# Kernel optimization log

Hardware: AMD Instinct MI355X
Metric: run time of the kernel (lower is better)

The kernel has to match this reference:

```python
import jax, jax.numpy as jnp
import numpy as np

B, S, D, H, F = 4, 1024, 2048, 16, 8192
HD = D // H  # head dim = 128
EPS = 1e-5


def layer_norm(x, w, b):
    mu = jnp.mean(x, axis=-1, keepdims=True)
    var = jnp.mean(jnp.square(x - mu), axis=-1, keepdims=True)
    return (x - mu) * jax.lax.rsqrt(var + EPS) * w + b


def setup_inputs() -> dict:
    key = jax.random.key(0)
    ks = jax.random.split(key, 12)
    s = 0.02  # realistic init scale for weights
    return {
        "x": jax.random.normal(ks[0], (B, S, D), jnp.float32),
        "attention_mask": jnp.zeros((B, 1, 1, S), jnp.float32),
        "wq": jax.random.normal(ks[1], (D, D), jnp.float32) * s,
        "bq": jax.random.normal(ks[2], (D,), jnp.float32) * s,
        "wk": jax.random.normal(ks[3], (D, D), jnp.float32) * s,
        "bk": jax.random.normal(ks[4], (D,), jnp.float32) * s,
        "wv": jax.random.normal(ks[5], (D, D), jnp.float32) * s,
        "bv": jax.random.normal(ks[6], (D,), jnp.float32) * s,
        "wo": jax.random.normal(ks[7], (D, D), jnp.float32) * s,
        "bo": jax.random.normal(ks[8], (D,), jnp.float32) * s,
        "ln1_w": jnp.ones((D,), jnp.float32),
        "ln1_b": jnp.zeros((D,), jnp.float32),
        "wi": jax.random.normal(ks[9], (F, D), jnp.float32) * s,
        "bi": jax.random.normal(ks[10], (F,), jnp.float32) * s,
        "wo2": jax.random.normal(ks[11], (D, F), jnp.float32) * s,
        "bo2": jnp.zeros((D,), jnp.float32),
        "ln2_w": jnp.ones((D,), jnp.float32),
        "ln2_b": jnp.zeros((D,), jnp.float32),
    }


def reference(x, attention_mask, wq, bq, wk, bk, wv, bv, wo, bo,
              ln1_w, ln1_b, wi, bi, wo2, bo2, ln2_w, ln2_b):
    # --- self attention ---
    q = (jnp.einsum('bsd,ed->bse', x, wq) + bq).reshape(B, S, H, HD).transpose(0, 2, 1, 3)
    k = (jnp.einsum('bsd,ed->bse', x, wk) + bk).reshape(B, S, H, HD).transpose(0, 2, 1, 3)
    v = (jnp.einsum('bsd,ed->bse', x, wv) + bv).reshape(B, S, H, HD).transpose(0, 2, 1, 3)
    scores = jnp.einsum('bhqd,bhkd->bhqk', q, k) / jnp.sqrt(jnp.float32(HD))
    scores = scores + attention_mask  # additive mask, broadcast over heads/query
    probs = jax.nn.softmax(scores, axis=-1)
    ctx = jnp.einsum('bhqk,bhkd->bhqd', probs, v)
    ctx = ctx.transpose(0, 2, 1, 3).reshape(B, S, D)
    # --- attention output: dense + bias + residual + LayerNorm ---
    attn_out = layer_norm(jnp.einsum('bsd,ed->bse', ctx, wo) + bo + x, ln1_w, ln1_b)
    # --- FFN: intermediate dense + bias, GELU, output dense + bias + residual + LN ---
    inter = jnp.einsum('bsd,fd->bsf', attn_out, wi) + bi
    h = jax.nn.gelu(inter, approximate=False)
    out = layer_norm(jnp.einsum('bsf,df->bsd', h, wo2) + bo2 + attn_out, ln2_w, ln2_b)
    return out
```

## Files before the change

### kernel.cpp

```cpp
#include <hip/hip_runtime.h>
#include <hip/hip_bf16.h>
#include <cstdint>
#include <cstddef>

typedef __attribute__((ext_vector_type(8))) short short8;
typedef __attribute__((ext_vector_type(4))) float f32x4;

#define DEV static __device__ __forceinline__

constexpr int kS = 1024, kD = 2048, kH = 16, kHD = 128, kF = 8192;
constexpr int kM = 4096;
constexpr int kDQKV = 6144;
constexpr float kEPS = 1e-5f;

constexpr size_t SZ_DD   = (size_t)kD * kD * 2;
constexpr size_t SZ_FD   = (size_t)kF * kD * 2;
constexpr size_t SZ_MD16 = (size_t)kM * kD * 2;
constexpr size_t SZ_MD32 = (size_t)kM * kD * 4;
constexpr size_t OFF_WQ  = 0;
constexpr size_t OFF_WK  = OFF_WQ + SZ_DD;
constexpr size_t OFF_WV  = OFF_WK + SZ_DD;
constexpr size_t OFF_WO  = OFF_WV + SZ_DD;
constexpr size_t OFF_WI  = OFF_WO + SZ_DD;
constexpr size_t OFF_WO2 = OFF_WI + SZ_FD;
constexpr size_t OFF_XB  = OFF_WO2 + SZ_FD;
constexpr size_t OFF_Q   = OFF_XB + SZ_MD16;
constexpr size_t OFF_H   = OFF_XB;
constexpr size_t OFF_CTX = OFF_Q + 3 * SZ_MD16;
constexpr size_t OFF_Y1  = OFF_CTX + SZ_MD16;
constexpr size_t OFF_A1B = OFF_Y1 + SZ_MD32;
constexpr size_t OFF_Y2  = OFF_A1B + SZ_MD16;
constexpr size_t WS_NEED = OFF_Y2 + SZ_MD32;

DEV void gload16(const void* g, void* l) {
  __builtin_amdgcn_global_load_lds(
      (const __attribute__((address_space(1))) unsigned int*)g,
      (__attribute__((address_space(3))) unsigned int*)l, 16, 0, 0);
}

DEV float b2f(short s) {
  union { unsigned u; float f; } x;
  x.u = ((unsigned)(unsigned short)s) << 16;
  return x.f;
}

__global__ void cvt_all(const float* __restrict__ x,  const float* __restrict__ wq,
                        const float* __restrict__ wk, const float* __restrict__ wv,
                        const float* __restrict__ bq, const float* __restrict__ bk,
                        const float* __restrict__ bv,
                        __hip_bfloat16* __restrict__ outw, float* __restrict__ bqkv) {
  constexpr int M1 = 1 << 20;
  constexpr int NW = 5 * M1;
  int stride = gridDim.x * blockDim.x;
  for (int i = blockIdx.x * blockDim.x + threadIdx.x; i < NW + 1536; i += stride) {
    if (i < NW) {
      const float* src; int off; int dst;
      if (i < 3 * M1) { src = (i < M1) ? wq : (i < 2 * M1) ? wk : wv;
                        off = i & (M1 - 1); dst = i; }
      else            { src = x; off = i - 3 * M1; dst = i + 9 * M1; }
      float4 v = reinterpret_cast<const float4*>(src)[off];
      union { ushort4 u; __hip_bfloat16 h[4]; } o;
      o.h[0] = __float2bfloat16(v.x);
      o.h[1] = __float2bfloat16(v.y);
      o.h[2] = __float2bfloat16(v.z);
      o.h[3] = __float2bfloat16(v.w);
      reinterpret_cast<ushort4*>(outw)[dst] = o.u;
    } else {
      int j = i - NW;
      const float* src = (j < 512) ? bq : (j < 1024) ? bk : bv;
      reinterpret_cast<float4*>(bqkv)[j] =
          reinterpret_cast<const float4*>(src)[j & 511];
    }
  }
}

template <int MODE>
__global__ __launch_bounds__(512, 2)
void gemm256(const __hip_bfloat16* __restrict__ A,
             const __hip_bfloat16* __restrict__ Bt,
             const float* __restrict__ bias,
             __hip_bfloat16* __restrict__ out0, __hip_bfloat16* __restrict__ out1,
             void* __restrict__ outb,
             int M, int N, int K, int kLen) {
  __shared__ __align__(16) char lds[131072];
  const int tid = threadIdx.x;
  const int lane = tid & 63, w = tid >> 6;
  const int wm = w >> 2, wn = w & 3;
  const int hw = w >> 2;
  const int lg = lane >> 4, lr = lane & 15;
  const int gy = M >> 8, gx = N >> 8;
  const int nwg = gridDim.x, orig = blockIdx.x;
  const int l = (orig & 7) * (nwg >> 3) + (orig >> 3);
  const int tilesPer = gx * gy;
  const int spl = l / tilesPer;
  const int rem = l - spl * tilesPer;
  const int bx = rem / gy, by = rem - bx * gy;
  const int m0 = by * 256, n0 = bx * 256;
  const int k0 = spl * kLen;
  const int NT = kLen >> 6;

  const char* gs[8];
  #pragma unroll
  for (int h = 0; h < 4; ++h) {
    const __hip_bfloat16* src = (h < 2) ? A : Bt;
    const int r0 = ((h < 2) ? m0 : n0) + (h & 1) * 128;
    #pragma unroll
    for (int i = 0; i < 2; ++i) {
      int c = i * 512 + tid;
      int row = c >> 3, slot = c & 7;
      gs[h * 2 + i] =
          (const char*)(src + (size_t)(r0 + row) * K + k0 + (slot ^ (row & 7)) * 8);
    }
  }

#define STAGE(P, H, TOFF)                                                          \
  {                                                                                \
    char* dstb = lds + (((H) < 2) ? 0 : 65536) + (P) * 32768 + ((H) & 1) * 16384;  \
    gload16(gs[(H) * 2 + 0] + (TOFF) * 128, dstb + (0 * 512 + tid) * 16);          \
    gload16(gs[(H) * 2 + 1] + (TOFF) * 128, dstb + (1 * 512 + tid) * 16);          \
  }

  auto ldA = [&](int P, int qm, int mr, int kk) {
    int row = qm * 128 + wm * 64 + mr * 16 + lr;
    return *reinterpret_cast<const short8*>(
        lds + P * 32768 + row * 128 + (((kk * 4 + lg) ^ (row & 7)) * 16));
  };
  auto ldB = [&](int P, int qn, int nr, int kk) {
    int row = qn * 128 + wn * 32 + nr * 16 + lr;
    return *reinterpret_cast<const short8*>(
        lds + 65536 + P * 32768 + row * 128 + (((kk * 4 + lg) ^ (row & 7)) * 16));
  };

  f32x4 acc[4][4][2] = {};

#define MFMA_HALF(p, kk, B)                                                     \
  _Pragma("unroll")                                                             \
  for (int mi = 0; mi < 4; ++mi)                                                \
    _Pragma("unroll")                                                           \
    for (int ni = 0; ni < 2; ++ni)                                              \
      acc[p][mi][ni] = __builtin_amdgcn_mfma_f32_16x16x32_bf16(                 \
          av[kk][mi], B[kk][ni], acc[p][mi][ni], 0, 0, 0);

#define WAIT_LGKM(n)                                                            \
  asm volatile("s_waitcnt lgkmcnt(" #n ")" ::: "memory");                       \
  __builtin_amdgcn_sched_barrier(0);

#define TILE_BODY(P, PF)                                                        \
  {                                                                             \
    asm volatile("s_waitcnt vmcnt(0)" ::: "memory");                            \
    __builtin_amdgcn_s_barrier();                                               \
    _Pragma("unroll")                                                           \
    for (int i = 0; i < 4; ++i) av[0][i] = ldA(P, hw, i, 0);                    \
    _Pragma("unroll")                                                           \
    for (int i = 0; i < 2; ++i) b0[0][i] = ldB(P, hw, i, 0);                    \
    _Pragma("unroll")                                                           \
    for (int i = 0; i < 4; ++i) av[1][i] = ldA(P, hw, i, 1);                    \
    _Pragma("unroll")                                                           \
    for (int i = 0; i < 2; ++i) b0[1][i] = ldB(P, hw, i, 1);                    \
    if (PF) { STAGE((P) ^ 1, 0, 1 + (P)) STAGE((P) ^ 1, 2, 1 + (P)) }           \
    WAIT_LGKM(6)                                                                \
    __builtin_amdgcn_s_setprio(1);                                              \
    MFMA_HALF(0, 0, b0)                                                         \
    WAIT_LGKM(0)                                                                \
    MFMA_HALF(0, 1, b0)                                                         \
    __builtin_amdgcn_s_setprio(0);                                              \
    _Pragma("unroll")                                                           \
    for (int i = 0; i < 2; ++i) b1[0][i] = ldB(P, 1 - hw, i, 0);                \
    _Pragma("unroll")                                                           \
    for (int i = 0; i < 2; ++i) b1[1][i] = ldB(P, 1 - hw, i, 1);                \
    if (PF) { STAGE((P) ^ 1, 3, 1 + (P)) STAGE((P) ^ 1, 1, 1 + (P)) }           \
    WAIT_LGKM(2)                                                                \
    __builtin_amdgcn_s_setprio(1);                                              \
    MFMA_HALF(1, 0, b1)                                                         \
    WAIT_LGKM(0)                                                                \
    MFMA_HALF(1, 1, b1)                                                         \
    __builtin_amdgcn_s_setprio(0);                                              \
    _Pragma("unroll")                                                           \
    for (int i = 0; i < 4; ++i) av[0][i] = ldA(P, 1 - hw, i, 0);                \
    _Pragma("unroll")                                                           \
    for (int i = 0; i < 4; ++i) av[1][i] = ldA(P, 1 - hw, i, 1);                \
    WAIT_LGKM(4)                                                                \
    __builtin_amdgcn_s_setprio(1);                                              \
    MFMA_HALF(2, 0, b1)                                                         \
    WAIT_LGKM(0)                                                                \
    MFMA_HALF(2, 1, b1)                                                         \
    __builtin_amdgcn_s_setprio(0);                                              \
    _Pragma("unroll")                                                           \
    for (int i = 0; i < 2; ++i) b0[0][i] = ldB(P, hw, i, 0);                    \
    _Pragma("unroll")                                                           \
    for (int i = 0; i < 2; ++i) b0[1][i] = ldB(P, hw, i, 1);                    \
    WAIT_LGKM(2)                                                                \
    __builtin_amdgcn_s_setprio(1);                                              \
    MFMA_HALF(3, 0, b0)                                                         \
    WAIT_LGKM(0)                                                                \
    MFMA_HALF(3, 1, b0)                                                         \
    __builtin_amdgcn_s_setprio(0);                                              \
  }

  STAGE(0, 0, 0) STAGE(0, 2, 0) STAGE(0, 3, 0) STAGE(0, 1, 0)

  for (int t2 = 0; t2 < NT; t2 += 2) {
    short8 av[2][4], b0[2][2], b1[2][2];
    TILE_BODY(0, true)
    TILE_BODY(1, (t2 + 2 < NT))
    #pragma unroll
    for (int j = 0; j < 8; ++j) gs[j] += 256;
  }
#undef TILE_BODY
#undef MFMA_HALF
#undef WAIT_LGKM
#undef STAGE

  #pragma unroll
  for (int p = 0; p < 4; ++p) {
    const int qm = (p < 2) ? hw : 1 - hw;
    const int qn = (p == 0 || p == 3) ? hw : 1 - hw;
    #pragma unroll
    for (int ni = 0; ni < 2; ++ni) {
      int col = n0 + qn * 128 + wn * 32 + ni * 16 + lr;
      float bvv = 0.f;
      if constexpr (MODE != 3) bvv = bias[col];
      #pragma unroll
      for (int mi = 0; mi < 4; ++mi) {
        int row0 = m0 + qm * 128 + wm * 64 + mi * 16 + lg * 4;
        #pragma unroll
        for (int r = 0; r < 4; ++r) {
          int row = row0 + r;
          float val = acc[p][mi][ni][r] + bvv;
          if constexpr (MODE == 0) {
            ((__hip_bfloat16*)outb)[(size_t)row * N + col] = __float2bfloat16(val);
          } else if constexpr (MODE == 2) {
            float g = 0.5f * val * (1.0f + erff(val * 0.70710678118654752f));
            ((__hip_bfloat16*)outb)[(size_t)row * N + col] = __float2bfloat16(g);
          } else {
            __hip_bfloat16* o = spl ? out1 : out0;
            o[(size_t)row * N + col] = __float2bfloat16(val);
          }
        }
      }
    }
  }
}

__global__ __launch_bounds__(512, 2)
void attn_fwd(const __hip_bfloat16* __restrict__ qkv,
              const float* __restrict__ mask,
              __hip_bfloat16* __restrict__ ctx,
              const float* __restrict__ wo,
              const float* __restrict__ wi, const float* __restrict__ wo2,
              __hip_bfloat16* __restrict__ outw ) {
  __shared__ __align__(16) char Ks[2][64 * 256];
  __shared__ __align__(16) char Vt[2][128 * 128];
  __shared__ __align__(16) char Ps[8][2048];
  const int tid = threadIdx.x, lane = tid & 63, w = tid >> 6;
  const int lg = lane >> 4, lr = lane & 15;
  const int orig = blockIdx.x;
  const int l = (orig & 7) * 32 + (orig >> 3);
  const int qp = l & 3, bh = l >> 2;
  const int b = bh >> 4, h = bh & 15;
  const int s4 = tid >> 5, hd4 = tid & 31;
  const size_t rb = (size_t)b * kS;
  const int hc = h * kHD;

  short8 qf[2][4];
  #pragma unroll
  for (int s = 0; s < 2; ++s) {
    const __hip_bfloat16* qp_ =
        qkv + (rb + qp * 256 + s * 128 + w * 16 + lr) * kDQKV + hc + lg * 8;
    #pragma unroll
    for (int kk = 0; kk < 4; ++kk)
      qf[s][kk] = *reinterpret_cast<const short8*>(qp_ + kk * 32);
  }

  auto stageK = [&](int bufi, int t) {
    #pragma unroll
    for (int i = 0; i < 2; ++i) {
      int c = i * 512 + tid;
      int row = c >> 4, slot = c & 15;
      gload16(qkv + (rb + t * 64 + row) * kDQKV + kD + hc + (slot ^ (row & 15)) * 8,
              Ks[bufi] + c * 16);
    }
  };
  union VU { uint2 u; ushort s[4]; };
  VU vr[4];
  auto loadV = [&](int t) {
    #pragma unroll
    for (int i = 0; i < 4; ++i)
      vr[i].u = *reinterpret_cast<const uint2*>(
          qkv + (rb + t * 64 + s4 * 4 + i) * kDQKV + 2 * kD + hc + hd4 * 4);
  };
  auto writeV = [&](int bufi) {
    #pragma unroll
    for (int j = 0; j < 4; ++j) {
      int hd = hd4 * 4 + j;
      ushort4 o4;
      o4.x = vr[0].s[j]; o4.y = vr[1].s[j]; o4.z = vr[2].s[j]; o4.w = vr[3].s[j];
      *reinterpret_cast<ushort4*>(
          Vt[bufi] + hd * 128 + (((s4 >> 1) ^ (hd & 7)) << 4) + ((s4 & 1) << 3)) = o4;
    }
  };
  float4 cw[4]; float4 cwo;
  auto cvLoad = [&](int t) {
    int g0 = ((orig * 16 + t) * 512 + tid) * 4;
    #pragma unroll
    for (int j = 0; j < 4; ++j) {
      int g = g0 + j;
      const float* src = (g < (4 << 20)) ? wi : wo2;
      int off = g & ((4 << 20) - 1);
      cw[j] = reinterpret_cast<const float4*>(src)[off];
    }
    int slot = (orig * 16 + t) * 512 + tid;
    if (slot < (1 << 20)) cwo = reinterpret_cast<const float4*>(wo)[slot];
  };
  auto cvStore = [&](int t) {
    int g0 = ((orig * 16 + t) * 512 + tid) * 4;
    #pragma unroll
    for (int j = 0; j < 4; ++j) {
      union { ushort4 u; __hip_bfloat16 hh[4]; } o4;
      o4.hh[0] = __float2bfloat16(cw[j].x);
      o4.hh[1] = __float2bfloat16(cw[j].y);
      o4.hh[2] = __float2bfloat16(cw[j].z);
      o4.hh[3] = __float2bfloat16(cw[j].w);
      reinterpret_cast<ushort4*>(outw)[(4 << 20) + g0 + j] = o4.u;
    }
    int slot = (orig * 16 + t) * 512 + tid;
    if (slot < (1 << 20)) {
      union { ushort4 u; __hip_bfloat16 hh[4]; } o4;
      o4.hh[0] = __float2bfloat16(cwo.x);
      o4.hh[1] = __float2bfloat16(cwo.y);
      o4.hh[2] = __float2bfloat16(cwo.z);
      o4.hh[3] = __float2bfloat16(cwo.w);
      reinterpret_cast<ushort4*>(outw)[(3 << 20) + slot] = o4.u;
    }
  };

  f32x4 o[2][8] = {};
  float mrun[2][4], lrun[2][4];
  #pragma unroll
  for (int s = 0; s < 2; ++s)
    #pragma unroll
    for (int r = 0; r < 4; ++r) { mrun[s][r] = -1e30f; lrun[s][r] = 0.f; }
  const float scale = 0.08838834764831845f;

  stageK(0, 0);
  loadV(0);
  writeV(0);
  __syncthreads();

  int buf = 0;
  for (int t = 0; t < 16; ++t) {
    if (t + 1 < 16) { stageK(buf ^ 1, t + 1); loadV(t + 1); }
    cvLoad(t);

    float mv[4];
    #pragma unroll
    for (int j = 0; j < 4; ++j) mv[j] = mask[(size_t)b * kS + t * 64 + j * 16 + lr];

    #pragma unroll
    for (int s = 0; s < 2; ++s) {
      f32x4 sacc[4] = {};
      #pragma unroll
      for (int j = 0; j < 4; ++j) {
        int key = j * 16 + lr;
        #pragma unroll
        for (int kk = 0; kk < 4; ++kk) {
          short8 bfrag = *reinterpret_cast<const short8*>(
              Ks[buf] + key * 256 + (((kk * 4 + lg) ^ (key & 15)) * 16));
          sacc[j] = __builtin_amdgcn_mfma_f32_16x16x32_bf16(qf[s][kk], bfrag, sacc[j], 0, 0, 0);
        }
      }
      float sarr[4][4];
      #pragma unroll
      for (int j = 0; j < 4; ++j)
        #pragma unroll
        for (int r = 0; r < 4; ++r) sarr[j][r] = sacc[j][r] * scale + mv[j];
      #pragma unroll
      for (int r = 0; r < 4; ++r) {
        float tm = fmaxf(fmaxf(sarr[0][r], sarr[1][r]), fmaxf(sarr[2][r], sarr[3][r]));
        #pragma unroll
        for (int d = 1; d < 16; d <<= 1) tm = fmaxf(tm, __shfl_xor(tm, d));
        float mnew = fmaxf(mrun[s][r], tm);
        float alpha = __expf(mrun[s][r] - mnew);
        mrun[s][r] = mnew;
        float rs = 0.f;
        #pragma unroll
        for (int j = 0; j < 4; ++j) {
          float p = __expf(sarr[j][r] - mnew);
          sarr[j][r] = p;
          rs += p;
        }
        #pragma unroll
        for (int d = 1; d < 16; d <<= 1) rs += __shfl_xor(rs, d);
        lrun[s][r] = lrun[s][r] * alpha + rs;
        #pragma unroll
        for (int n = 0; n < 8; ++n) o[s][n][r] *= alpha;
      }
      #pragma unroll
      for (int r = 0; r < 4; ++r) {
        int qr = lg * 4 + r;
        #pragma unroll
        for (int j = 0; j < 4; ++j)
          *reinterpret_cast<__hip_bfloat16*>(
              Ps[w] + ((qr * 128 + (j * 16 + lr) * 2) ^ ((qr & 7) << 4))) =
              __float2bfloat16(sarr[j][r]);
      }
      #pragma unroll
      for (int kk2 = 0; kk2 < 2; ++kk2) {
        short8 pa = *reinterpret_cast<const short8*>(
            Ps[w] + ((lr * 128 + kk2 * 64 + lg * 16) ^ ((lr & 7) << 4)));
        #pragma unroll
        for (int n = 0; n < 8; ++n) {
          int hd = n * 16 + lr;
          short8 vb = *reinterpret_cast<const short8*>(
              Vt[buf] + hd * 128 + (((kk2 * 4 + lg) ^ (hd & 7)) * 16));
          o[s][n] = __builtin_amdgcn_mfma_f32_16x16x32_bf16(pa, vb, o[s][n], 0, 0, 0);
        }
      }
    }
    cvStore(t);
    if (t + 1 < 16) writeV(buf ^ 1);
    __syncthreads();
    buf ^= 1;
  }

  #pragma unroll
  for (int s = 0; s < 2; ++s)
    #pragma unroll
    for (int r = 0; r < 4; ++r) {
      float inv = 1.0f / lrun[s][r];
      int srow = qp * 256 + s * 128 + w * 16 + lg * 4 + r;
      __hip_bfloat16* cp = ctx + (rb + srow) * kD + hc + lr;
      #pragma unroll
      for (int n = 0; n < 8; ++n) cp[n * 16] = __float2bfloat16(o[s][n][r] * inv);
    }
}

template <bool F32OUT>
__global__ void ln_fuse(const __hip_bfloat16* __restrict__ p0,
                        const __hip_bfloat16* __restrict__ p1,
                        const float* __restrict__ bias,
                        const __hip_bfloat16* __restrict__ res,
                        const float* __restrict__ w, const float* __restrict__ b,
                        float* __restrict__ outf, __hip_bfloat16* __restrict__ outb) {
  const int row = blockIdx.x, tid = threadIdx.x;
  const size_t base = (size_t)row * kD;
  short8 a = reinterpret_cast<const short8*>(p0 + base)[tid];
  short8 c = reinterpret_cast<const short8*>(p1 + base)[tid];
  short8 rr = reinterpret_cast<const short8*>(res + base)[tid];
  float v[8];
  #pragma unroll
  for (int i = 0; i < 2; ++i) {
    int c4 = tid * 2 + i;
    float4 bs = reinterpret_cast<const float4*>(bias)[c4];
    v[i * 4 + 0] = b2f(a[i * 4 + 0]) + b2f(c[i * 4 + 0]) + b2f(rr[i * 4 + 0]) + bs.x;
    v[i * 4 + 1] = b2f(a[i * 4 + 1]) + b2f(c[i * 4 + 1]) + b2f(rr[i * 4 + 1]) + bs.y;
    v[i * 4 + 2] = b2f(a[i * 4 + 2]) + b2f(c[i * 4 + 2]) + b2f(rr[i * 4 + 2]) + bs.z;
    v[i * 4 + 3] = b2f(a[i * 4 + 3]) + b2f(c[i * 4 + 3]) + b2f(rr[i * 4 + 3]) + bs.w;
  }
  float s = 0.f;
  #pragma unroll
  for (int i = 0; i < 8; ++i) s += v[i];
  #pragma unroll
  for (int off = 32; off > 0; off >>= 1) s += __shfl_down(s, off);
  __shared__ float r1[4], r2[4];
  if ((tid & 63) == 0) r1[tid >> 6] = s;
  __syncthreads();
  float mean = (r1[0] + r1[1] + r1[2] + r1[3]) * (1.0f / kD);
  float qv = 0.f;
  #pragma unroll
  for (int i = 0; i < 8; ++i) { float d = v[i] - mean; qv += d * d; }
  #pragma unroll
  for (int off = 32; off > 0; off >>= 1) qv += __shfl_down(qv, off);
  if ((tid & 63) == 0) r2[tid >> 6] = qv;
  __syncthreads();
  float rstd = rsqrtf((r2[0] + r2[1] + r2[2] + r2[3]) * (1.0f / kD) + kEPS);
  #pragma unroll
  for (int i = 0; i < 8; ++i) {
    int col = tid * 8 + i;
    float ov = (v[i] - mean) * rstd * w[col] + b[col];
    if constexpr (F32OUT) outf[base + col] = ov;
    else                  outb[base + col] = __float2bfloat16(ov);
  }
}

extern "C" void kernel_launch(void* const* d_in, const int* in_sizes, int n_in,
                              void* d_out, int out_size, void* d_ws, size_t ws_size,
                              hipStream_t stream) {
  (void)in_sizes; (void)n_in; (void)out_size;
  if (ws_size < WS_NEED) return;
  const float* x    = (const float*)d_in[0];
  const float* mask = (const float*)d_in[1];
  const float* wq   = (const float*)d_in[2];
  const float* bq   = (const float*)d_in[3];
  const float* wk   = (const float*)d_in[4];
  const float* bk   = (const float*)d_in[5];
  const float* wv   = (const float*)d_in[6];
  const float* bv   = (const float*)d_in[7];
  const float* wo   = (const float*)d_in[8];
  const float* bo   = (const float*)d_in[9];
  const float* l1w  = (const float*)d_in[10];
  const float* l1b  = (const float*)d_in[11];
  const float* wi   = (const float*)d_in[12];
  const float* bi   = (const float*)d_in[13];
  const float* wo2  = (const float*)d_in[14];
  const float* bo2  = (const float*)d_in[15];
  const float* l2w  = (const float*)d_in[16];
  const float* l2b  = (const float*)d_in[17];

  char* ws = (char*)d_ws;
  __hip_bfloat16* wqb  = (__hip_bfloat16*)(ws + OFF_WQ);
  __hip_bfloat16* wob  = (__hip_bfloat16*)(ws + OFF_WO);
  __hip_bfloat16* wib  = (__hip_bfloat16*)(ws + OFF_WI);
  __hip_bfloat16* wo2b = (__hip_bfloat16*)(ws + OFF_WO2);
  __hip_bfloat16* xb   = (__hip_bfloat16*)(ws + OFF_XB);
  __hip_bfloat16* qkvb = (__hip_bfloat16*)(ws + OFF_Q);
  __hip_bfloat16* hb   = (__hip_bfloat16*)(ws + OFF_H);
  __hip_bfloat16* ctxb = (__hip_bfloat16*)(ws + OFF_CTX);
  __hip_bfloat16* a1b  = (__hip_bfloat16*)(ws + OFF_A1B);
  __hip_bfloat16* wp0 = (__hip_bfloat16*)(ws + OFF_Y2);
  __hip_bfloat16* wp1 = (__hip_bfloat16*)(ws + OFF_Y2 + SZ_MD16);
  __hip_bfloat16* fp0 = (__hip_bfloat16*)(ws + OFF_WQ);
  __hip_bfloat16* fp1 = (__hip_bfloat16*)(ws + OFF_WQ + SZ_MD16);
  float* bqkv = (float*)(ws + OFF_Y2);

  cvt_all<<<2048, 256, 0, stream>>>(x, wq, wk, wv, bq, bk, bv, wqb, bqkv);

  dim3 blk(512);
  gemm256<0><<<dim3(384), blk, 0, stream>>>(
      xb, wqb, bqkv, nullptr, nullptr, qkvb, kM, kDQKV, kD, kD);
  attn_fwd<<<dim3(256), dim3(512), 0, stream>>>(qkvb, mask, ctxb, wo, wi, wo2, wqb);
  gemm256<3><<<dim3(256), blk, 0, stream>>>(
      ctxb, wob, nullptr, wp0, wp1, nullptr, kM, kD, kD, kD / 2);
  ln_fuse<false><<<kM, 256, 0, stream>>>(wp0, wp1, bo, xb, l1w, l1b, nullptr, a1b);
  gemm256<2><<<dim3(512), blk, 0, stream>>>(
      a1b, wib, bi, nullptr, nullptr, hb, kM, kF, kD, kD);
  gemm256<3><<<dim3(256), blk, 0, stream>>>(
      hb, wo2b, nullptr, fp0, fp1, nullptr, kM, kD, kF, kF / 2);
  ln_fuse<true><<<kM, 256, 0, stream>>>(fp0, fp1, bo2, a1b, l2w, l2b, (float*)d_out, nullptr);
}
```

Baseline: 555.1 us.

## Restructure GEMM main loop into barrier-synchronized phases with per-stage vmcnt waits

Replaces the staggered per-wave-half quadrant ordering (hw) with a uniform quadrant order for all waves. The per-tile vmcnt(0) wait becomes four phases, each bracketed by workgroup barriers, with a finer vmcnt wait so each prefetch stage overlaps the MFMA work of the following phases. The aim is to hide global-load latency better and keep all waves in lockstep on LDS reads. The cost is more s_barrier instructions per tile, and dropping the half-wave stagger may add LDS bank or issue contention.

```diff
diff --git a/kernel.cpp b/kernel.cpp
--- a/kernel.cpp
+++ b/kernel.cpp
@@ -86,7 +86,6 @@
   const int tid = threadIdx.x;
   const int lane = tid & 63, w = tid >> 6;
   const int wm = w >> 2, wn = w & 3;
-  const int hw = w >> 2;
   const int lg = lane >> 4, lr = lane & 15;
   const int gy = M >> 8, gx = N >> 8;
   const int nwg = gridDim.x, orig = blockIdx.x;
@@ -133,71 +132,67 @@
 
   f32x4 acc[4][4][2] = {};
 
-#define MFMA_HALF(p, kk, B)                                                     \
+#define MFMA_QUAD(q, B)                                                         \
   _Pragma("unroll")                                                             \
-  for (int mi = 0; mi < 4; ++mi)                                                \
-    _Pragma("unroll")                                                           \
-    for (int ni = 0; ni < 2; ++ni)                                              \
-      acc[p][mi][ni] = __builtin_amdgcn_mfma_f32_16x16x32_bf16(                 \
-          av[kk][mi], B[kk][ni], acc[p][mi][ni], 0, 0, 0);
-
-#define WAIT_LGKM(n)                                                            \
-  asm volatile("s_waitcnt lgkmcnt(" #n ")" ::: "memory");                       \
-  __builtin_amdgcn_sched_barrier(0);
+  for (int kk = 0; kk < 2; ++kk)                                                \
+    _Pragma("unroll")                                                           \
+    for (int mi = 0; mi < 4; ++mi)                                              \
+      _Pragma("unroll")                                                         \
+      for (int ni = 0; ni < 2; ++ni)                                            \
+        acc[q][mi][ni] = __builtin_amdgcn_mfma_f32_16x16x32_bf16(               \
+            av[kk][mi], B[kk][ni], acc[q][mi][ni], 0, 0, 0);
+
+#define VM(n) asm volatile("s_waitcnt vmcnt(" #n ")" ::: "memory");
+
+#define PHASE_CORE(Q, B, WAITSTMT)                                              \
+    __builtin_amdgcn_s_barrier();                                               \
+    asm volatile("s_waitcnt lgkmcnt(0)" ::: "memory");                          \
+    __builtin_amdgcn_sched_barrier(0);                                          \
+    __builtin_amdgcn_s_setprio(1);                                              \
+    MFMA_QUAD(Q, B)                                                             \
+    __builtin_amdgcn_s_setprio(0);                                              \
+    WAITSTMT                                                                    \
+    __builtin_amdgcn_s_barrier();
 
 #define TILE_BODY(P, PF)                                                        \
   {                                                                             \
-    asm volatile("s_waitcnt vmcnt(0)" ::: "memory");                            \
-    __builtin_amdgcn_s_barrier();                                               \
-    _Pragma("unroll")                                                           \
-    for (int i = 0; i < 4; ++i) av[0][i] = ldA(P, hw, i, 0);                    \
-    _Pragma("unroll")                                                           \
-    for (int i = 0; i < 2; ++i) b0[0][i] = ldB(P, hw, i, 0);                    \
-    _Pragma("unroll")                                                           \
-    for (int i = 0; i < 4; ++i) av[1][i] = ldA(P, hw, i, 1);                    \
-    _Pragma("unroll")                                                           \
-    for (int i = 0; i < 2; ++i) b0[1][i] = ldB(P, hw, i, 1);                    \
-    if (PF) { STAGE((P) ^ 1, 0, 1 + (P)) STAGE((P) ^ 1, 2, 1 + (P)) }           \
-    WAIT_LGKM(6)                                                                \
-    __builtin_amdgcn_s_setprio(1);                                              \
-    MFMA_HALF(0, 0, b0)                                                         \
-    WAIT_LGKM(0)                                                                \
-    MFMA_HALF(0, 1, b0)                                                         \
-    __builtin_amdgcn_s_setprio(0);                                              \
-    _Pragma("unroll")                                                           \
-    for (int i = 0; i < 2; ++i) b1[0][i] = ldB(P, 1 - hw, i, 0);                \
-    _Pragma("unroll")                                                           \
-    for (int i = 0; i < 2; ++i) b1[1][i] = ldB(P, 1 - hw, i, 1);                \
-    if (PF) { STAGE((P) ^ 1, 3, 1 + (P)) STAGE((P) ^ 1, 1, 1 + (P)) }           \
-    WAIT_LGKM(2)                                                                \
-    __builtin_amdgcn_s_setprio(1);                                              \
-    MFMA_HALF(1, 0, b1)                                                         \
-    WAIT_LGKM(0)                                                                \
-    MFMA_HALF(1, 1, b1)                                                         \
-    __builtin_amdgcn_s_setprio(0);                                              \
-    _Pragma("unroll")                                                           \
-    for (int i = 0; i < 4; ++i) av[0][i] = ldA(P, 1 - hw, i, 0);                \
-    _Pragma("unroll")                                                           \
-    for (int i = 0; i < 4; ++i) av[1][i] = ldA(P, 1 - hw, i, 1);                \
-    WAIT_LGKM(4)                                                                \
-    __builtin_amdgcn_s_setprio(1);                                              \
-    MFMA_HALF(2, 0, b1)                                                         \
-    WAIT_LGKM(0)                                                                \
-    MFMA_HALF(2, 1, b1)                                                         \
-    __builtin_amdgcn_s_setprio(0);                                              \
-    _Pragma("unroll")                                                           \
-    for (int i = 0; i < 2; ++i) b0[0][i] = ldB(P, hw, i, 0);                    \
-    _Pragma("unroll")                                                           \
-    for (int i = 0; i < 2; ++i) b0[1][i] = ldB(P, hw, i, 1);                    \
-    WAIT_LGKM(2)                                                                \
-    __builtin_amdgcn_s_setprio(1);                                              \
-    MFMA_HALF(3, 0, b0)                                                         \
-    WAIT_LGKM(0)                                                                \
-    MFMA_HALF(3, 1, b0)                                                         \
-    __builtin_amdgcn_s_setprio(0);                                              \
+                  \
+    _Pragma("unroll")                                                           \
+    for (int i = 0; i < 4; ++i) av[0][i] = ldA(P, 0, i, 0);                     \
+    _Pragma("unroll")                                                           \
+    for (int i = 0; i < 2; ++i) b0[0][i] = ldB(P, 0, i, 0);                     \
+    _Pragma("unroll")                                                           \
+    for (int i = 0; i < 4; ++i) av[1][i] = ldA(P, 0, i, 1);                     \
+    _Pragma("unroll")                                                           \
+    for (int i = 0; i < 2; ++i) b0[1][i] = ldB(P, 0, i, 1);                     \
+    if (PF) STAGE((P) ^ 1, 0, 1 + (P))                                          \
+    if (PF) { PHASE_CORE(0, b0, VM(4)) } else { PHASE_CORE(0, b0, VM(2)) }      \
+          \
+    _Pragma("unroll")                                                           \
+    for (int i = 0; i < 2; ++i) b1[0][i] = ldB(P, 1, i, 0);                     \
+    _Pragma("unroll")                                                           \
+    for (int i = 0; i < 2; ++i) b1[1][i] = ldB(P, 1, i, 1);                     \
+    if (PF) STAGE((P) ^ 1, 2, 1 + (P))                                          \
+    if (PF) { PHASE_CORE(1, b1, VM(4)) } else { PHASE_CORE(1, b1, VM(0)) }      \
+                         \
+    _Pragma("unroll")                                                           \
+    for (int i = 0; i < 4; ++i) av[0][i] = ldA(P, 1, i, 0);                     \
+    _Pragma("unroll")                                                           \
+    for (int i = 0; i < 4; ++i) av[1][i] = ldA(P, 1, i, 1);                     \
+    if (PF) STAGE((P) ^ 1, 3, 1 + (P))                                          \
+    PHASE_CORE(2, b1, )                                                         \
+     \
+    _Pragma("unroll")                                                           \
+    for (int i = 0; i < 2; ++i) b0[0][i] = ldB(P, 0, i, 0);                     \
+    _Pragma("unroll")                                                           \
+    for (int i = 0; i < 2; ++i) b0[1][i] = ldB(P, 0, i, 1);                     \
+    if (PF) STAGE((P) ^ 1, 1, 1 + (P))                                          \
+    if (PF) { PHASE_CORE(3, b0, VM(4)) } else { PHASE_CORE(3, b0, ) }           \
   }
 
   STAGE(0, 0, 0) STAGE(0, 2, 0) STAGE(0, 3, 0) STAGE(0, 1, 0)
+  VM(4)
+  __builtin_amdgcn_s_barrier();
 
   for (int t2 = 0; t2 < NT; t2 += 2) {
     short8 av[2][4], b0[2][2], b1[2][2];
@@ -207,14 +202,15 @@
     for (int j = 0; j < 8; ++j) gs[j] += 256;
   }
 #undef TILE_BODY
-#undef MFMA_HALF
-#undef WAIT_LGKM
+#undef PHASE_CORE
+#undef MFMA_QUAD
+#undef VM
 #undef STAGE
 
   #pragma unroll
   for (int p = 0; p < 4; ++p) {
-    const int qm = (p < 2) ? hw : 1 - hw;
-    const int qn = (p == 0 || p == 3) ? hw : 1 - hw;
+    const int qm = (p >= 2) ? 1 : 0;
+    const int qn = (p == 1 || p == 2) ? 1 : 0;
     #pragma unroll
     for (int ni = 0; ni < 2; ++ni) {
       int col = n0 + qn * 128 + wn * 32 + ni * 16 + lr;
```

Result: slower. 850.6 us (+53.2%).
